# Performance work log

Hardware: AMD Instinct MI355X
Metric: run time of the kernel (lower is better)

Reference implementation:

```python
import jax, jax.numpy as jnp
import numpy as np

B, T = 256, 50
N_ITEMS = 100000
EMB = 256      # embedding
KBD = 128      # KBembedding == MN_dims
HID = 256      # layers[0] == layers[-1]
OUT = 256      # out_dim
NF = 10        # MN_nfactors == n_r


def setup_inputs() -> dict:
    key = jax.random.key(0)
    ks = jax.random.split(key, 18)
    s = 0.05
    return {
        "X": jax.random.randint(ks[0], (B, T), 0, N_ITEMS),
        "E": jax.random.normal(ks[1], (N_ITEMS, EMB), jnp.float32) * s,
        "KBE": jax.random.normal(ks[2], (N_ITEMS, KBD), jnp.float32) * s,
        "r_matrix": jax.random.normal(ks[3], (NF, KBD), jnp.float32) * s,
        "W_ih": jax.random.normal(ks[4], (3 * HID, EMB), jnp.float32) * s,
        "W_hh": jax.random.normal(ks[5], (3 * HID, HID), jnp.float32) * s,
        "b_ih": jnp.zeros((3 * HID,), jnp.float32),
        "b_hh": jnp.zeros((3 * HID,), jnp.float32),
        "MNu_W": jax.random.normal(ks[6], (KBD, HID), jnp.float32) * s,
        "MNu_b": jnp.zeros((KBD,), jnp.float32),
        "MNu2_W": jax.random.normal(ks[7], (HID, KBD + HID), jnp.float32) * s,
        "MNu2_b": jnp.zeros((HID,), jnp.float32),
        "MNea_W": jax.random.normal(ks[8], (KBD, KBD), jnp.float32) * s,
        "MNea_b": jnp.zeros((KBD,), jnp.float32),
        "mlp1_W": jax.random.normal(ks[9], (OUT, HID), jnp.float32) * s,
        "mlp1_b": jnp.zeros((OUT,), jnp.float32),
        "mlp2_W": jax.random.normal(ks[10], (OUT, EMB + KBD), jnp.float32) * s,
        "mlp2_b": jnp.zeros((OUT,), jnp.float32),
    }


def _gru_cell(x, h, W_ih, W_hh, b_ih, b_hh):
    # PyTorch GRUCell: gates stacked [r, z, n] along dim 0 of weights
    gi = x @ W_ih.T + b_ih
    gh = h @ W_hh.T + b_hh
    ir, iz, inn = jnp.split(gi, 3, axis=-1)
    hr, hz, hn = jnp.split(gh, 3, axis=-1)
    r = jax.nn.sigmoid(ir + hr)
    z = jax.nn.sigmoid(iz + hz)
    n = jnp.tanh(inn + r * hn)
    return (1.0 - z) * n + z * h


def reference(X, E, KBE, r_matrix, W_ih, W_hh, b_ih, b_hh,
              MNu_W, MNu_b, MNu2_W, MNu2_b, MNea_W, MNea_b,
              mlp1_W, mlp1_b, mlp2_W, mlp2_b):
    Bv, Tv = X.shape
    Em = E.at[0].set(0.0)     # mask row 0 of E
    KBm = KBE.at[0].set(0.0)  # mask row 0 of KBE
    Sx = Em[X]                # (B, T, EMB)
    KBItem = KBm[X]           # (B, T, KBD)

    def step(carry, xs):
        h, MN, y_sum = carry
        x_t, kb_t = xs                      # (B, EMB), (B, KBD)
        h = _gru_cell(x_t, h, W_ih, W_hh, b_ih, b_hh)
        y = h                                # dropout p=0 -> identity
        # gated memory write
        EA = jnp.tanh(kb_t @ MNea_W.T + MNea_b)          # (B, KBD)
        EA = EA[:, None, :] + r_matrix                    # (B, NF, KBD)
        gate = jax.nn.sigmoid(jnp.sum(MN * EA, axis=-1, keepdims=True))  # (B, NF, 1)
        MN = MN * (1.0 - gate) + EA * gate
        # attention read
        U = jnp.tanh(y @ MNu_W.T + MNu_b)                 # (B, KBD)
        AW = jax.nn.softmax(U @ r_matrix.T, axis=1)       # (B, NF)
        AC = jnp.einsum('bfd,bf->bd', MN, AW)             # (B, KBD)
        Ut = jnp.tanh(jnp.concatenate([y, AC], axis=-1) @ MNu2_W.T + MNu2_b)  # (B, HID)
        y_out = jnp.tanh(Ut @ mlp1_W.T + mlp1_b)          # (B, OUT)
        return (h, MN, y_sum + y_out), None

    init = (jnp.zeros((Bv, HID), Sx.dtype),
            jnp.zeros((Bv, NF, KBD), Sx.dtype),
            jnp.zeros((Bv, OUT), Sx.dtype))
    xs = (jnp.swapaxes(Sx, 0, 1), jnp.swapaxes(KBItem, 0, 1))  # (T, B, *)
    (h, MN, y_sum), _ = jax.lax.scan(step, init, xs)
    y = y_sum / Tv

    MergeE = jnp.concatenate([E, KBE], axis=1).at[0].set(0.0)  # (N, EMB+KBD)
    Sy = jnp.tanh(MergeE @ mlp2_W.T + mlp2_b)                  # (N, OUT)
    scores = jax.nn.log_softmax(y @ Sy.T, axis=1)              # (B, N)
    return scores, y
```

## Files before the change

kernel.cpp:

```cpp
#include <hip/hip_runtime.h>

typedef _Float16 f16;
typedef _Float16 f16x8 __attribute__((ext_vector_type(8)));
typedef float f32x4 __attribute__((ext_vector_type(4)));

#define MFMA16(a,b,c) __builtin_amdgcn_mfma_f32_16x16x32_f16(a,b,c,0,0,0)

#define NITEMS 100000
#define NBLK4  1563

#define OFF_WIH   0u
#define OFF_WHH   393216u
#define OFF_MNU   786432u
#define OFF_MNU2  851968u
#define OFF_MNEA  1048576u
#define OFF_MLP1  1081344u
#define OFF_MLP2  1212416u
#define OFF_GI    1409024u
#define OFF_TV    21069824u
#define OFF_MN    24346624u
#define OFF_YALL  57114624u
#define OFF_SY    66945024u
#define OFF_Y16   118407168u
#define OFF_PMAX  118538240u
#define OFF_PSUM  120176640u
#define OFF_LSE   121815040u

__device__ __forceinline__ float sigm(float x) { return 1.f / (1.f + __expf(-x)); }
__device__ __forceinline__ float tanh_fast(float x) {
  return 1.f - 2.f / (1.f + __expf(2.f * x));
}

__global__ __launch_bounds__(256) void k_pack(
    const float* s0, const float* s1, const float* s2, const float* s3,
    const float* s4, const float* s5, const float* s6, f16* base)
{
  int fid = blockIdx.x * 256 + threadIdx.x;
  const float* src; f16* dst; int K, f;
  if (fid < 24576)      { src = s0; dst = base;          K = 256; f = fid; }
  else if (fid < 49152) { src = s1; dst = base + 196608; K = 256; f = fid - 24576; }
  else if (fid < 53248) { src = s2; dst = base + 393216; K = 256; f = fid - 49152; }
  else if (fid < 65536) { src = s3; dst = base + 425984; K = 384; f = fid - 53248; }
  else if (fid < 67584) { src = s4; dst = base + 524288; K = 128; f = fid - 65536; }
  else if (fid < 75776) { src = s5; dst = base + 540672; K = 256; f = fid - 67584; }
  else                  { src = s6; dst = base + 606208; K = 384; f = fid - 75776; }
  int lane = f & 63, t2 = f >> 6, KS = K >> 5;
  int ks = t2 % KS, nt = t2 / KS;
  int row = nt * 16 + (lane & 15), col = ks * 32 + ((lane >> 4) << 3);
  const float* sp = src + (size_t)row * K + col;
  f16x8 v;
  #pragma unroll
  for (int j = 0; j < 8; j++) v[j] = (f16)sp[j];
  *(f16x8*)(dst + (size_t)f * 8) = v;
}

__global__ __launch_bounds__(512) void k_giea(
    const int* __restrict__ X, const float* __restrict__ E,
    const f16* __restrict__ Wih_p, const float* __restrict__ bih, f16* __restrict__ gi,
    const float* __restrict__ KBE, const f16* __restrict__ Wea_p,
    const float* __restrict__ bea, f16* __restrict__ tv)
{
  __shared__ __align__(16) f16 At[32][264];
  int tid = threadIdx.x;
  int w = tid >> 6, lane = tid & 63, lr = lane & 15, lg = lane >> 4;
  if (blockIdx.x < 400) {
    int r0 = blockIdx.x * 32;
    int t = r0 >> 8;
    {
      int r = tid >> 4, c = (tid & 15) * 16;
      int b = (r0 + r) & 255;
      int item = X[b * 50 + t];
      if (item == 0) {
        #pragma unroll
        for (int j = 0; j < 16; j++) At[r][c + j] = (f16)0.f;
      } else {
        const float4* sp = (const float4*)(E + (size_t)item * 256 + c);
        #pragma unroll
        for (int q = 0; q < 4; q++) {
          float4 v = sp[q];
          At[r][c + q*4 + 0] = (f16)v.x; At[r][c + q*4 + 1] = (f16)v.y;
          At[r][c + q*4 + 2] = (f16)v.z; At[r][c + q*4 + 3] = (f16)v.w;
        }
      }
    }
    __syncthreads();
    f32x4 acc[2][6] = {};
    for (int ks = 0; ks < 8; ks++) {
      f16x8 a0 = *(const f16x8*)(&At[lr][ks * 32 + lg * 8]);
      f16x8 a1 = *(const f16x8*)(&At[16 + lr][ks * 32 + lg * 8]);
      #pragma unroll
      for (int j = 0; j < 6; j++) {
        int nt = w * 6 + j;
        f16x8 bf = *(const f16x8*)(Wih_p + ((size_t)((nt * 8 + ks) * 64 + lane) << 3));
        acc[0][j] = MFMA16(a0, bf, acc[0][j]);
        acc[1][j] = MFMA16(a1, bf, acc[1][j]);
      }
    }
    #pragma unroll
    for (int j = 0; j < 6; j++) {
      int col = (w * 6 + j) * 16 + lr;
      float bias = bih[col];
      #pragma unroll
      for (int mt = 0; mt < 2; mt++)
        #pragma unroll
        for (int rr = 0; rr < 4; rr++) {
          int row = r0 + mt * 16 + lg * 4 + rr;
          gi[(size_t)row * 768 + col] = (f16)(acc[mt][j][rr] + bias);
        }
    }
  } else {
    int r0 = (blockIdx.x - 400) * 32;
    int t = r0 >> 8;
    {
      int r = tid >> 4, c = (tid & 15) * 8;
      int b = (r0 + r) & 255;
      int item = X[b * 50 + t];
      if (item == 0) {
        #pragma unroll
        for (int j = 0; j < 8; j++) At[r][c + j] = (f16)0.f;
      } else {
        const float4* sp = (const float4*)(KBE + (size_t)item * 128 + c);
        #pragma unroll
        for (int q = 0; q < 2; q++) {
          float4 v = sp[q];
          At[r][c + q*4 + 0] = (f16)v.x; At[r][c + q*4 + 1] = (f16)v.y;
          At[r][c + q*4 + 2] = (f16)v.z; At[r][c + q*4 + 3] = (f16)v.w;
        }
      }
    }
    __syncthreads();
    f32x4 acc[2] = {};
    for (int ks = 0; ks < 4; ks++) {
      f16x8 a0 = *(const f16x8*)(&At[lr][ks * 32 + lg * 8]);
      f16x8 a1 = *(const f16x8*)(&At[16 + lr][ks * 32 + lg * 8]);
      f16x8 bf = *(const f16x8*)(Wea_p + ((size_t)((w * 4 + ks) * 64 + lane) << 3));
      acc[0] = MFMA16(a0, bf, acc[0]);
      acc[1] = MFMA16(a1, bf, acc[1]);
    }
    int col = w * 16 + lr;
    float bias = bea[col];
    #pragma unroll
    for (int mt = 0; mt < 2; mt++)
      #pragma unroll
      for (int rr = 0; rr < 4; rr++) {
        int row = r0 + mt * 16 + lg * 4 + rr;
        tv[(size_t)row * 128 + col] = (f16)tanh_fast(acc[mt][rr] + bias);
      }
  }
}

__global__ __launch_bounds__(1024)
__attribute__((amdgpu_waves_per_eu(4, 4)))
void k_fused(
    const f16* __restrict__ Whh_p, const float* __restrict__ bhh,
    const f16* __restrict__ gi, f16* __restrict__ y_all,
    const f16* __restrict__ tv, const float* __restrict__ Rm, f16* __restrict__ MN,
    const float* __restrict__ E, const float* __restrict__ KBE,
    const f16* __restrict__ mlp2_p, const float* __restrict__ mlp2b, f16* __restrict__ Sy)
{
  __shared__ __align__(16) char smem[147456];
  int tid = threadIdx.x, w = tid >> 6, lane = tid & 63, lr = lane & 15, lg = lane >> 4;

  if (blockIdx.x < 32) {
    f16* Wlds = (f16*)smem;
    f16* hb0 = (f16*)(smem + 131072);
    f16* hb1 = (f16*)(smem + 139264);
    int r0 = blockIdx.x * 8;
    {
      const float4* src = (const float4*)Whh_p;
      float4* dst = (float4*)Wlds;
      #pragma unroll
      for (int i = 0; i < 8; i++) dst[tid + i * 1024] = src[tid + i * 1024];
      float4 z4 = {0.f, 0.f, 0.f, 0.f};
      ((float4*)hb0)[tid] = z4;
    }
    f16x8 Wz[8], Wn[8];
    #pragma unroll
    for (int ks = 0; ks < 8; ks++) {
      Wz[ks] = *(const f16x8*)(Whh_p + ((size_t)(((16 + w) * 8 + ks) * 64 + lane) << 3));
      Wn[ks] = *(const f16x8*)(Whh_p + ((size_t)(((32 + w) * 8 + ks) * 64 + lane) << 3));
      asm volatile("" : "+a"(Wz[ks]), "+a"(Wn[ks]));
    }
    int col = w * 16 + lr;
    float bR = bhh[col], bZ = bhh[col + 256], bN = bhh[col + 512];
    float hreg[4] = {0.f, 0.f, 0.f, 0.f};
    const f16* gP = gi + (size_t)(r0 + lg * 4) * 768 + col;
    f16 P[4][3];
    if (lg < 2) {
      #pragma unroll
      for (int rr = 0; rr < 4; rr++)
        #pragma unroll
        for (int g = 0; g < 3; g++)
          P[rr][g] = gP[rr * 768 + g * 256];
    }
    __syncthreads();
    f16* hc = hb0; f16* hn_ = hb1;
    int xr = (lr & 7) << 4;
    const f16* wB0 = Wlds + (size_t)w * 4096 + lane * 8;
    for (int t = 0; t < 50; t++) {
      f32x4 aR = {}, aZ = {}, aN = {};
      const char* hbase = (const char*)hc + lr * 512;
      #pragma unroll
      for (int ks = 0; ks < 8; ks++) {
        f16x8 a = *(const f16x8*)(hbase + ((ks * 64 + lg * 16) ^ xr));
        aR = MFMA16(a, *(const f16x8*)(wB0 + ks * 512), aR);
        aZ = MFMA16(a, Wz[ks], aZ);
        aN = MFMA16(a, Wn[ks], aN);
      }
      if (lg < 2) {
        #pragma unroll
        for (int rr = 0; rr < 4; rr++) {
          int row = lg * 4 + rr;
          float rg = sigm((float)P[rr][0] + aR[rr] + bR);
          float zg = sigm((float)P[rr][1] + aZ[rr] + bZ);
          float ng = tanh_fast((float)P[rr][2] + rg * (aN[rr] + bN));
          float hv = ng + zg * (hreg[rr] - ng);
          hreg[rr] = hv;
          *(f16*)((char*)hn_ + row * 512 + ((col * 2) ^ ((row & 7) << 4))) = (f16)hv;
        }
        if (t < 49) {
          const f16* gN = gP + (size_t)(t + 1) * 196608;
          #pragma unroll
          for (int rr = 0; rr < 4; rr++)
            #pragma unroll
            for (int g = 0; g < 3; g++)
              P[rr][g] = gN[rr * 768 + g * 256];
        }
      }
      __syncthreads();
      if (tid < 256) {
        int row = tid >> 5, c = tid & 31;
        f16x8 hv = *(const f16x8*)((char*)hn_ + row * 512 + ((c * 16) ^ ((row & 7) << 4)));
        *(f16x8*)(y_all + ((size_t)t * 256 + r0 + row) * 256 + c * 8) = hv;
      }
      f16* tmp = hc; hc = hn_; hn_ = tmp;
    }
  } else if (blockIdx.x < 192) {
    int pair = (blockIdx.x - 32) * 16 + w;
    int b = pair / 10, f = pair - (pair / 10) * 10;
    float r0_ = Rm[f * 128 + lane], r1_ = Rm[f * 128 + 64 + lane];
    float mn0 = 0.f, mn1 = 0.f;
    for (int t = 0; t < 50; t++) {
      size_t base = ((size_t)t * 256 + b) * 128;
      float ea0 = (float)tv[base + lane] + r0_;
      float ea1 = (float)tv[base + 64 + lane] + r1_;
      float p = mn0 * ea0 + mn1 * ea1;
      #pragma unroll
      for (int off = 32; off > 0; off >>= 1) p += __shfl_xor(p, off);
      float g = sigm(p);
      mn0 += (ea0 - mn0) * g;
      mn1 += (ea1 - mn1) * g;
      size_t mb = (((size_t)t * 256 + b) * 10 + f) * 128;
      MN[mb + lane] = (f16)mn0;
      MN[mb + 64 + lane] = (f16)mn1;
    }
  } else {
    f16* At = (f16*)smem;
    int i0 = (blockIdx.x - 192) * 32;
    {
      int r = tid >> 5;
      int item = i0 + r;
      int c = (tid & 31) * 8;
      if (item == 0) {
        #pragma unroll
        for (int j = 0; j < 8; j++) At[r * 392 + c + j] = (f16)0.f;
      } else {
        const float4* sp = (const float4*)(E + (size_t)item * 256 + c);
        #pragma unroll
        for (int q = 0; q < 2; q++) {
          float4 v = sp[q];
          At[r * 392 + c + q*4 + 0] = (f16)v.x; At[r * 392 + c + q*4 + 1] = (f16)v.y;
          At[r * 392 + c + q*4 + 2] = (f16)v.z; At[r * 392 + c + q*4 + 3] = (f16)v.w;
        }
      }
      int c2 = (tid & 31) * 4;
      if (item == 0) {
        #pragma unroll
        for (int j = 0; j < 4; j++) At[r * 392 + 256 + c2 + j] = (f16)0.f;
      } else {
        float4 v = *(const float4*)(KBE + (size_t)item * 128 + c2);
        At[r * 392 + 256 + c2 + 0] = (f16)v.x; At[r * 392 + 256 + c2 + 1] = (f16)v.y;
        At[r * 392 + 256 + c2 + 2] = (f16)v.z; At[r * 392 + 256 + c2 + 3] = (f16)v.w;
      }
    }
    __syncthreads();
    int mt = w & 1, ntp = w >> 1;
    f32x4 acc[2] = {};
    for (int ks = 0; ks < 12; ks++) {
      f16x8 a = *(const f16x8*)(&At[(mt * 16 + lr) * 392 + ks * 32 + lg * 8]);
      #pragma unroll
      for (int j = 0; j < 2; j++) {
        int nt = ntp * 2 + j;
        f16x8 bf = *(const f16x8*)(mlp2_p + ((size_t)((nt * 12 + ks) * 64 + lane) << 3));
        acc[j] = MFMA16(a, bf, acc[j]);
      }
    }
    #pragma unroll
    for (int j = 0; j < 2; j++) {
      int col = (ntp * 2 + j) * 16 + lr;
      float bias = mlp2b[col];
      #pragma unroll
      for (int rr = 0; rr < 4; rr++) {
        int item = i0 + mt * 16 + lg * 4 + rr;
        Sy[(size_t)item * 256 + col] = (f16)tanh_fast(acc[j][rr] + bias);
      }
    }
  }
}

__global__ __launch_bounds__(512) void k_uacut(
    const f16* __restrict__ y_all, const f16* __restrict__ MNu_p,
    const float* __restrict__ MNub, const float* __restrict__ Rm,
    const f16* __restrict__ MN,
    const f16* __restrict__ MNu2_p, const float* __restrict__ MNu2b,
    const f16* __restrict__ mlp1_p, const float* __restrict__ mlp1b,
    float* __restrict__ ypart)
{
  __shared__ __align__(16) char smem[25088];
  int tid = threadIdx.x, w = tid >> 6, lane = tid & 63, lr = lane & 15, lg = lane >> 4;
  f16   (*Aty)[264] = (f16(*)[264])smem;
  float (*Uf)[136]  = (float(*)[136])(smem + 8448);
  f16   (*Utl)[264] = (f16(*)[264])(smem + 8448);
  float (*Lg)[10]   = (float(*)[10])(smem + 17152);
  float (*Aw)[10]   = (float(*)[10])(smem + 17792);
  f16   (*ACs)[136] = (f16(*)[136])(smem + 18432);
  int r0 = blockIdx.x * 16;
  {
    int r = tid >> 5, c = (tid & 31) * 8;
    f16x8 v = *(const f16x8*)(y_all + (size_t)(r0 + r) * 256 + c);
    *(f16x8*)(&Aty[r][c]) = v;
  }
  __syncthreads();
  {
    f32x4 acc = {};
    for (int ks = 0; ks < 8; ks++) {
      f16x8 a = *(const f16x8*)(&Aty[lr][ks * 32 + lg * 8]);
      f16x8 bf = *(const f16x8*)(MNu_p + ((size_t)((w * 8 + ks) * 64 + lane) << 3));
      acc = MFMA16(a, bf, acc);
    }
    int col = w * 16 + lr;
    float bias = MNub[col];
    #pragma unroll
    for (int rr = 0; rr < 4; rr++)
      Uf[lg * 4 + rr][col] = tanh_fast(acc[rr] + bias);
  }
  __syncthreads();
  if (tid < 160) {
    int row = tid / 10, f = tid - (tid / 10) * 10;
    float s = 0.f;
    for (int d = 0; d < 128; d++) s += Uf[row][d] * Rm[f * 128 + d];
    Lg[row][f] = s;
  }
  __syncthreads();
  if (tid < 16) {
    float m = -1e30f;
    #pragma unroll
    for (int f = 0; f < 10; f++) m = fmaxf(m, Lg[tid][f]);
    float e[10], s = 0.f;
    #pragma unroll
    for (int f = 0; f < 10; f++) { e[f] = __expf(Lg[tid][f] - m); s += e[f]; }
    float inv = 1.f / s;
    #pragma unroll
    for (int f = 0; f < 10; f++) Aw[tid][f] = e[f] * inv;
  }
  __syncthreads();
  if (tid < 256) {
    int row = tid >> 4, d0 = (tid & 15) * 8;
    float a[8] = {0,0,0,0,0,0,0,0};
    for (int f = 0; f < 10; f++) {
      float wgt = Aw[row][f];
      f16x8 mv = *(const f16x8*)(MN + (((size_t)(r0 + row)) * 10 + f) * 128 + d0);
      #pragma unroll
      for (int q = 0; q < 8; q++) a[q] += wgt * (float)mv[q];
    }
    f16x8 o;
    #pragma unroll
    for (int q = 0; q < 8; q++) o[q] = (f16)a[q];
    *(f16x8*)(&ACs[row][d0]) = o;
  }
  __syncthreads();
  {
    f32x4 acc[2] = {};
    for (int ks = 0; ks < 12; ks++) {
      f16x8 a = (ks < 8)
        ? *(const f16x8*)(&Aty[lr][ks * 32 + lg * 8])
        : *(const f16x8*)(&ACs[lr][(ks - 8) * 32 + lg * 8]);
      #pragma unroll
      for (int j = 0; j < 2; j++) {
        f16x8 bf = *(const f16x8*)(MNu2_p + ((size_t)(((w * 2 + j) * 12 + ks) * 64 + lane) << 3));
        acc[j] = MFMA16(a, bf, acc[j]);
      }
    }
    __syncthreads();
    #pragma unroll
    for (int j = 0; j < 2; j++) {
      int col = (w * 2 + j) * 16 + lr;
      float bias = MNu2b[col];
      #pragma unroll
      for (int rr = 0; rr < 4; rr++)
        Utl[lg * 4 + rr][col] = (f16)tanh_fast(acc[j][rr] + bias);
    }
  }
  __syncthreads();
  {
    f32x4 acc2[2] = {};
    for (int ks = 0; ks < 8; ks++) {
      f16x8 a = *(const f16x8*)(&Utl[lr][ks * 32 + lg * 8]);
      #pragma unroll
      for (int j = 0; j < 2; j++) {
        f16x8 bf = *(const f16x8*)(mlp1_p + ((size_t)(((w * 2 + j) * 8 + ks) * 64 + lane) << 3));
        acc2[j] = MFMA16(a, bf, acc2[j]);
      }
    }
    #pragma unroll
    for (int j = 0; j < 2; j++) {
      int col = (w * 2 + j) * 16 + lr;
      float bias = mlp1b[col];
      #pragma unroll
      for (int rr = 0; rr < 4; rr++) {
        int row = r0 + lg * 4 + rr;
        ypart[(size_t)row * 256 + col] = tanh_fast(acc2[j][rr] + bias);
      }
    }
  }
}

__global__ __launch_bounds__(256) void k_yfin(
    const float* __restrict__ ypart, float* __restrict__ outy, f16* __restrict__ y16)
{
  int b = blockIdx.x, c = threadIdx.x;
  float s = 0.f;
  for (int t = 0; t < 50; t++) s += ypart[((size_t)t * 256 + b) * 256 + c];
  float v = s * (1.0f / 50.0f);
  outy[b * 256 + c] = v;
  y16[b * 256 + c] = (f16)v;
}

template <int FINAL>
__global__ __launch_bounds__(512) void k_scores(
    const f16* __restrict__ y16, const f16* __restrict__ Sy,
    const float* __restrict__ lse, float* __restrict__ pmax,
    float* __restrict__ psum, float* __restrict__ out)
{
  __shared__ __align__(16) char smx[FINAL ? 67584 : 4096];
  int tid = threadIdx.x, w = tid >> 6, lane = tid & 63, lr = lane & 15, lg = lane >> 4;
  int i0 = blockIdx.x * 64;
  int mtb = (w >> 1) * 4, ntb = (w & 1) * 2;
  f32x4 acc[4][2] = {};
  for (int ks = 0; ks < 8; ks++) {
    f16x8 a[4];
    #pragma unroll
    for (int i = 0; i < 4; i++)
      a[i] = *(const f16x8*)(y16 + ((size_t)((mtb + i) * 16 + lr)) * 256 + ks * 32 + lg * 8);
    #pragma unroll
    for (int j = 0; j < 2; j++) {
      int item = i0 + (ntb + j) * 16 + lr;
      int ic = item < NITEMS ? item : (NITEMS - 1);
      f16x8 bv = *(const f16x8*)(Sy + (size_t)ic * 256 + ks * 32 + lg * 8);
      #pragma unroll
      for (int i = 0; i < 4; i++) acc[i][j] = MFMA16(a[i], bv, acc[i][j]);
    }
  }
  if constexpr (!FINAL) {
    float* pm = (float*)smx;
    float* ps = (float*)(smx + 2048);
    int item0 = i0 + ntb * 16 + lr, item1 = item0 + 16;
    bool v0 = item0 < NITEMS, v1 = item1 < NITEMS;
    #pragma unroll
    for (int i = 0; i < 4; i++)
      #pragma unroll
      for (int rr = 0; rr < 4; rr++) {
        float x0 = v0 ? acc[i][0][rr] : -1e30f;
        float x1 = v1 ? acc[i][1][rr] : -1e30f;
        float m = fmaxf(x0, x1);
        m = fmaxf(m, __shfl_xor(m, 1)); m = fmaxf(m, __shfl_xor(m, 2));
        m = fmaxf(m, __shfl_xor(m, 4)); m = fmaxf(m, __shfl_xor(m, 8));
        float s = (v0 ? __expf(x0 - m) : 0.f) + (v1 ? __expf(x1 - m) : 0.f);
        s += __shfl_xor(s, 1); s += __shfl_xor(s, 2);
        s += __shfl_xor(s, 4); s += __shfl_xor(s, 8);
        if (lr == 0) {
          int row = (mtb + i) * 16 + lg * 4 + rr;
          pm[(w & 1) * 256 + row] = m;
          ps[(w & 1) * 256 + row] = s;
        }
      }
    __syncthreads();
    if (tid < 256) {
      float m0 = pm[tid], m1 = pm[256 + tid];
      float s0 = ps[tid], s1 = ps[256 + tid];
      float M = fmaxf(m0, m1);
      float S = s0 * __expf(m0 - M) + s1 * __expf(m1 - M);
      pmax[(size_t)tid * 1600 + blockIdx.x] = M;
      psum[(size_t)tid * 1600 + blockIdx.x] = S;
    }
  } else {
    float (*oS)[65] = (float(*)[65])smx;
    float* lse_s = (float*)(smx + 66560);
    if (tid < 256) lse_s[tid] = lse[tid];
    __syncthreads();
    #pragma unroll
    for (int i = 0; i < 4; i++)
      #pragma unroll
      for (int j = 0; j < 2; j++)
        #pragma unroll
        for (int rr = 0; rr < 4; rr++) {
          int row = (mtb + i) * 16 + lg * 4 + rr;
          int c = (ntb + j) * 16 + lr;
          oS[row][c] = acc[i][j][rr] - lse_s[row];
        }
    __syncthreads();
    for (int it = 0; it < 32; it++) {
      int row = it * 8 + (tid >> 6);
      int c = tid & 63;
      if (i0 + c < NITEMS) out[(size_t)row * NITEMS + i0 + c] = oS[row][c];
    }
  }
}

__global__ __launch_bounds__(256) void k_lse(
    const float* __restrict__ pmax, const float* __restrict__ psum, float* __restrict__ lse)
{
  int b = blockIdx.x, tid = threadIdx.x;
  __shared__ float red[256];
  float m = -1e30f;
  for (int i = tid; i < NBLK4; i += 256) m = fmaxf(m, pmax[(size_t)b * 1600 + i]);
  red[tid] = m; __syncthreads();
  for (int s = 128; s > 0; s >>= 1) {
    if (tid < s) red[tid] = fmaxf(red[tid], red[tid + s]);
    __syncthreads();
  }
  float M = red[0]; __syncthreads();
  float s = 0.f;
  for (int i = tid; i < NBLK4; i += 256)
    s += psum[(size_t)b * 1600 + i] * __expf(pmax[(size_t)b * 1600 + i] - M);
  red[tid] = s; __syncthreads();
  for (int q = 128; q > 0; q >>= 1) {
    if (tid < q) red[tid] += red[tid + q];
    __syncthreads();
  }
  if (tid == 0) lse[b] = M + logf(red[0]);
}

extern "C" void kernel_launch(void* const* d_in, const int* in_sizes, int n_in,
                              void* d_out, int out_size, void* d_ws, size_t ws_size,
                              hipStream_t stream) {
  (void)in_sizes; (void)n_in; (void)out_size; (void)ws_size;
  const int*   X     = (const int*)d_in[0];
  const float* E     = (const float*)d_in[1];
  const float* KBE   = (const float*)d_in[2];
  const float* Rm    = (const float*)d_in[3];
  const float* Wih   = (const float*)d_in[4];
  const float* Whh   = (const float*)d_in[5];
  const float* bih   = (const float*)d_in[6];
  const float* bhh   = (const float*)d_in[7];
  const float* MNuW  = (const float*)d_in[8];
  const float* MNub  = (const float*)d_in[9];
  const float* MNu2W = (const float*)d_in[10];
  const float* MNu2b = (const float*)d_in[11];
  const float* MNeaW = (const float*)d_in[12];
  const float* MNeab = (const float*)d_in[13];
  const float* mlp1W = (const float*)d_in[14];
  const float* mlp1b = (const float*)d_in[15];
  const float* mlp2W = (const float*)d_in[16];
  const float* mlp2b = (const float*)d_in[17];

  char* ws = (char*)d_ws;
  f16*   Wih_p  = (f16*)(ws + OFF_WIH);
  f16*   Whh_p  = (f16*)(ws + OFF_WHH);
  f16*   MNu_p  = (f16*)(ws + OFF_MNU);
  f16*   MNu2_p = (f16*)(ws + OFF_MNU2);
  f16*   Wea_p  = (f16*)(ws + OFF_MNEA);
  f16*   mlp1_p = (f16*)(ws + OFF_MLP1);
  f16*   mlp2_p = (f16*)(ws + OFF_MLP2);
  f16*   gi     = (f16*)(ws + OFF_GI);
  f16*   tv     = (f16*)(ws + OFF_TV);
  f16*   MN     = (f16*)(ws + OFF_MN);
  f16*   y_all  = (f16*)(ws + OFF_YALL);
  f16*   Sy     = (f16*)(ws + OFF_SY);
  float* ypart  = (float*)(ws + OFF_GI);
  f16*   y16    = (f16*)(ws + OFF_Y16);
  float* pmax   = (float*)(ws + OFF_PMAX);
  float* psum   = (float*)(ws + OFF_PSUM);
  float* lse    = (float*)(ws + OFF_LSE);
  float* outf   = (float*)d_out;

  k_pack<<<344, 256, 0, stream>>>(Wih, Whh, MNuW, MNu2W, MNeaW, mlp1W, mlp2W, (f16*)ws);
  k_giea<<<800, 512, 0, stream>>>(X, E, Wih_p, bih, gi, KBE, Wea_p, MNeab, tv);
  k_fused<<<3317, 1024, 0, stream>>>(Whh_p, bhh, gi, y_all, tv, Rm, MN,
                                     E, KBE, mlp2_p, mlp2b, Sy);
  k_uacut<<<800, 512, 0, stream>>>(y_all, MNu_p, MNub, Rm, MN,
                                   MNu2_p, MNu2b, mlp1_p, mlp1b, ypart);
  k_yfin<<<256, 256, 0, stream>>>(ypart, outf + 25600000, y16);
  k_scores<0><<<NBLK4, 512, 0, stream>>>(y16, Sy, nullptr, pmax, psum, nullptr);
  k_lse<<<256, 256, 0, stream>>>(pmax, psum, lse);
  k_scores<1><<<NBLK4, 512, 0, stream>>>(y16, Sy, lse, nullptr, nullptr, outf);
}
```

Before: 382.4 us.

## Make Sy tiles persistent with double buffering; compute scores once and fix up with LSE

The Sy projection part of the fused kernel becomes persistent. 224 blocks loop over tiles and prefetch the next tile's E/KBE rows into registers while the MFMA runs on a double-buffered LDS tile. The scores GEMM is now computed only once: raw logits are written to the output together with the partial max/sum, and a small k_fix kernel subtracts the log-sum-exp in place. This drops the second GEMM pass over Sy but adds an extra read and write of the full 100MB output.

```diff
diff --git a/kernel.cpp b/kernel.cpp
--- a/kernel.cpp
+++ b/kernel.cpp
@@ -255,55 +255,80 @@
       MN[mb + 64 + lane] = (f16)mn1;
     }
   } else {
-    f16* At = (f16*)smem;
-    int i0 = (blockIdx.x - 192) * 32;
+    f16* Ab0 = (f16*)smem;
+    f16* Ab1 = (f16*)(smem + 25088);
+    int bsy = blockIdx.x - 192;
+    int r = tid >> 5, cE = (tid & 31) * 8, cK = (tid & 31) * 4;
+    int mt = w & 1, ntp = w >> 1;
+    float eE[8], eK[4];
+    int tile = bsy;
     {
-      int r = tid >> 5;
-      int item = i0 + r;
-      int c = (tid & 31) * 8;
+      int item = tile * 32 + r;
       if (item == 0) {
         #pragma unroll
-        for (int j = 0; j < 8; j++) At[r * 392 + c + j] = (f16)0.f;
+        for (int j = 0; j < 8; j++) eE[j] = 0.f;
+        #pragma unroll
+        for (int j = 0; j < 4; j++) eK[j] = 0.f;
       } else {
-        const float4* sp = (const float4*)(E + (size_t)item * 256 + c);
-        #pragma unroll
-        for (int q = 0; q < 2; q++) {
-          float4 v = sp[q];
-          At[r * 392 + c + q*4 + 0] = (f16)v.x; At[r * 392 + c + q*4 + 1] = (f16)v.y;
-          At[r * 392 + c + q*4 + 2] = (f16)v.z; At[r * 392 + c + q*4 + 3] = (f16)v.w;
-        }
-      }
-      int c2 = (tid & 31) * 4;
-      if (item == 0) {
-        #pragma unroll
-        for (int j = 0; j < 4; j++) At[r * 392 + 256 + c2 + j] = (f16)0.f;
-      } else {
-        float4 v = *(const float4*)(KBE + (size_t)item * 128 + c2);
-        At[r * 392 + 256 + c2 + 0] = (f16)v.x; At[r * 392 + 256 + c2 + 1] = (f16)v.y;
-        At[r * 392 + 256 + c2 + 2] = (f16)v.z; At[r * 392 + 256 + c2 + 3] = (f16)v.w;
-      }
-    }
-    __syncthreads();
-    int mt = w & 1, ntp = w >> 1;
-    f32x4 acc[2] = {};
-    for (int ks = 0; ks < 12; ks++) {
-      f16x8 a = *(const f16x8*)(&At[(mt * 16 + lr) * 392 + ks * 32 + lg * 8]);
+        const float4* sp = (const float4*)(E + (size_t)item * 256 + cE);
+        float4 v0 = sp[0], v1 = sp[1];
+        eE[0]=v0.x; eE[1]=v0.y; eE[2]=v0.z; eE[3]=v0.w;
+        eE[4]=v1.x; eE[5]=v1.y; eE[6]=v1.z; eE[7]=v1.w;
+        float4 k0 = *(const float4*)(KBE + (size_t)item * 128 + cK);
+        eK[0]=k0.x; eK[1]=k0.y; eK[2]=k0.z; eK[3]=k0.w;
+      }
+    }
+    int cur = 0;
+    while (tile < 3125) {
+      f16* buf = cur ? Ab1 : Ab0;
+      {
+        f16* rowp = buf + r * 392;
+        #pragma unroll
+        for (int j = 0; j < 8; j++) rowp[cE + j] = (f16)eE[j];
+        #pragma unroll
+        for (int j = 0; j < 4; j++) rowp[256 + cK + j] = (f16)eK[j];
+      }
+      __syncthreads();
+      int nxt = tile + 224;
+      if (nxt < 3125) {
+        int item = nxt * 32 + r;
+        if (item == 0) {
+          #pragma unroll
+          for (int j = 0; j < 8; j++) eE[j] = 0.f;
+          #pragma unroll
+          for (int j = 0; j < 4; j++) eK[j] = 0.f;
+        } else {
+          const float4* sp = (const float4*)(E + (size_t)item * 256 + cE);
+          float4 v0 = sp[0], v1 = sp[1];
+          eE[0]=v0.x; eE[1]=v0.y; eE[2]=v0.z; eE[3]=v0.w;
+          eE[4]=v1.x; eE[5]=v1.y; eE[6]=v1.z; eE[7]=v1.w;
+          float4 k0 = *(const float4*)(KBE + (size_t)item * 128 + cK);
+          eK[0]=k0.x; eK[1]=k0.y; eK[2]=k0.z; eK[3]=k0.w;
+        }
+      }
+      int i0 = tile * 32;
+      f32x4 acc[2] = {};
+      for (int ks = 0; ks < 12; ks++) {
+        f16x8 a = *(const f16x8*)(buf + (mt * 16 + lr) * 392 + ks * 32 + lg * 8);
+        #pragma unroll
+        for (int j = 0; j < 2; j++) {
+          int nt = ntp * 2 + j;
+          f16x8 bf = *(const f16x8*)(mlp2_p + ((size_t)((nt * 12 + ks) * 64 + lane) << 3));
+          acc[j] = MFMA16(a, bf, acc[j]);
+        }
+      }
       #pragma unroll
       for (int j = 0; j < 2; j++) {
-        int nt = ntp * 2 + j;
-        f16x8 bf = *(const f16x8*)(mlp2_p + ((size_t)((nt * 12 + ks) * 64 + lane) << 3));
-        acc[j] = MFMA16(a, bf, acc[j]);
-      }
-    }
-    #pragma unroll
-    for (int j = 0; j < 2; j++) {
-      int col = (ntp * 2 + j) * 16 + lr;
-      float bias = mlp2b[col];
-      #pragma unroll
-      for (int rr = 0; rr < 4; rr++) {
-        int item = i0 + mt * 16 + lg * 4 + rr;
-        Sy[(size_t)item * 256 + col] = (f16)tanh_fast(acc[j][rr] + bias);
-      }
+        int colS = (ntp * 2 + j) * 16 + lr;
+        float bias = mlp2b[colS];
+        #pragma unroll
+        for (int rr = 0; rr < 4; rr++) {
+          int item = i0 + mt * 16 + lg * 4 + rr;
+          Sy[(size_t)item * 256 + colS] = (f16)tanh_fast(acc[j][rr] + bias);
+        }
+      }
+      __syncthreads();
+      tile = nxt; cur ^= 1;
     }
   }
 }
@@ -436,13 +461,11 @@
   y16[b * 256 + c] = (f16)v;
 }
 
-template <int FINAL>
-__global__ __launch_bounds__(512) void k_scores(
+__global__ __launch_bounds__(512) void k_scoreraw(
     const f16* __restrict__ y16, const f16* __restrict__ Sy,
-    const float* __restrict__ lse, float* __restrict__ pmax,
-    float* __restrict__ psum, float* __restrict__ out)
-{
-  __shared__ __align__(16) char smx[FINAL ? 67584 : 4096];
+    float* __restrict__ pmax, float* __restrict__ psum, float* __restrict__ out)
+{
+  __shared__ __align__(16) char smx[70656];
   int tid = threadIdx.x, w = tid >> 6, lane = tid & 63, lr = lane & 15, lg = lane >> 4;
   int i0 = blockIdx.x * 64;
   int mtb = (w >> 1) * 4, ntb = (w & 1) * 2;
@@ -461,9 +484,20 @@
       for (int i = 0; i < 4; i++) acc[i][j] = MFMA16(a[i], bv, acc[i][j]);
     }
   }
-  if constexpr (!FINAL) {
-    float* pm = (float*)smx;
-    float* ps = (float*)(smx + 2048);
+  float (*oS)[65] = (float(*)[65])smx;
+  float* pm = (float*)(smx + 66560);
+  float* ps = (float*)(smx + 68608);
+  #pragma unroll
+  for (int i = 0; i < 4; i++)
+    #pragma unroll
+    for (int j = 0; j < 2; j++)
+      #pragma unroll
+      for (int rr = 0; rr < 4; rr++) {
+        int row = (mtb + i) * 16 + lg * 4 + rr;
+        int c = (ntb + j) * 16 + lr;
+        oS[row][c] = acc[i][j][rr];
+      }
+  {
     int item0 = i0 + ntb * 16 + lr, item1 = item0 + 16;
     bool v0 = item0 < NITEMS, v1 = item1 < NITEMS;
     #pragma unroll
@@ -484,36 +518,20 @@
           ps[(w & 1) * 256 + row] = s;
         }
       }
-    __syncthreads();
-    if (tid < 256) {
-      float m0 = pm[tid], m1 = pm[256 + tid];
-      float s0 = ps[tid], s1 = ps[256 + tid];
-      float M = fmaxf(m0, m1);
-      float S = s0 * __expf(m0 - M) + s1 * __expf(m1 - M);
-      pmax[(size_t)tid * 1600 + blockIdx.x] = M;
-      psum[(size_t)tid * 1600 + blockIdx.x] = S;
-    }
-  } else {
-    float (*oS)[65] = (float(*)[65])smx;
-    float* lse_s = (float*)(smx + 66560);
-    if (tid < 256) lse_s[tid] = lse[tid];
-    __syncthreads();
-    #pragma unroll
-    for (int i = 0; i < 4; i++)
-      #pragma unroll
-      for (int j = 0; j < 2; j++)
-        #pragma unroll
-        for (int rr = 0; rr < 4; rr++) {
-          int row = (mtb + i) * 16 + lg * 4 + rr;
-          int c = (ntb + j) * 16 + lr;
-          oS[row][c] = acc[i][j][rr] - lse_s[row];
-        }
-    __syncthreads();
-    for (int it = 0; it < 32; it++) {
-      int row = it * 8 + (tid >> 6);
-      int c = tid & 63;
-      if (i0 + c < NITEMS) out[(size_t)row * NITEMS + i0 + c] = oS[row][c];
-    }
+  }
+  __syncthreads();
+  for (int it = 0; it < 32; it++) {
+    int row = it * 8 + (tid >> 6);
+    int c = tid & 63;
+    if (i0 + c < NITEMS) out[(size_t)row * NITEMS + i0 + c] = oS[row][c];
+  }
+  if (tid < 256) {
+    float m0 = pm[tid], m1 = pm[256 + tid];
+    float s0 = ps[tid], s1 = ps[256 + tid];
+    float M = fmaxf(m0, m1);
+    float S = s0 * __expf(m0 - M) + s1 * __expf(m1 - M);
+    pmax[(size_t)tid * 1600 + blockIdx.x] = M;
+    psum[(size_t)tid * 1600 + blockIdx.x] = S;
   }
 }
 
@@ -539,6 +557,20 @@
     __syncthreads();
   }
   if (tid == 0) lse[b] = M + logf(red[0]);
+}
+
+__global__ __launch_bounds__(256) void k_fix(
+    float* __restrict__ out, const float* __restrict__ lse)
+{
+  int row = blockIdx.y;
+  int idx = blockIdx.x * 256 + threadIdx.x;
+  if (idx < 25000) {
+    float l = lse[row];
+    float4* p = (float4*)(out + (size_t)row * NITEMS) + idx;
+    float4 v = *p;
+    v.x -= l; v.y -= l; v.z -= l; v.w -= l;
+    *p = v;
+  }
 }
 
 extern "C" void kernel_launch(void* const* d_in, const int* in_sizes, int n_in,
@@ -586,12 +618,13 @@
 
   k_pack<<<344, 256, 0, stream>>>(Wih, Whh, MNuW, MNu2W, MNeaW, mlp1W, mlp2W, (f16*)ws);
   k_giea<<<800, 512, 0, stream>>>(X, E, Wih_p, bih, gi, KBE, Wea_p, MNeab, tv);
-  k_fused<<<3317, 1024, 0, stream>>>(Whh_p, bhh, gi, y_all, tv, Rm, MN,
-                                     E, KBE, mlp2_p, mlp2b, Sy);
+  k_fused<<<416, 1024, 0, stream>>>(Whh_p, bhh, gi, y_all, tv, Rm, MN,
+                                    E, KBE, mlp2_p, mlp2b, Sy);
   k_uacut<<<800, 512, 0, stream>>>(y_all, MNu_p, MNub, Rm, MN,
                                    MNu2_p, MNu2b, mlp1_p, mlp1b, ypart);
   k_yfin<<<256, 256, 0, stream>>>(ypart, outf + 25600000, y16);
-  k_scores<0><<<NBLK4, 512, 0, stream>>>(y16, Sy, nullptr, pmax, psum, nullptr);
+  k_scoreraw<<<NBLK4, 512, 0, stream>>>(y16, Sy, pmax, psum, outf);
   k_lse<<<256, 256, 0, stream>>>(pmax, psum, lse);
-  k_scores<1><<<NBLK4, 512, 0, stream>>>(y16, Sy, lse, nullptr, nullptr, outf);
-}
+  dim3 gfix(98, 256);
+  k_fix<<<gfix, 256, 0, stream>>>(outf, lse);
+}
```

Result: no change. 383.5 us (+0.3%).
